# Optimization experiments

Hardware: AMD Instinct MI355X
Metric: run time of the kernel (lower is better)

The kernel has to match this reference:

```python
import jax, jax.numpy as jnp
import numpy as np

N_NODES = 100000
N_EDGES = 1000000
D = 128          # input_dim == hidden_dim (required: h = zeros_like(nh) accumulates src_nf)
OUT = 128
NUM_TYPES = 5


def setup_inputs() -> dict:
    key = jax.random.key(0)
    ks = jax.random.split(key, 7)
    nh = jax.random.normal(ks[0], (N_NODES, D), dtype=jnp.float32)
    edge_y = jax.random.randint(ks[1], (N_EDGES,), 0, NUM_TYPES, dtype=jnp.int64)
    edge_index = jax.random.randint(ks[2], (2, N_EDGES), 0, N_NODES, dtype=jnp.int64)
    # nn.Linear weights, scaled for numerical sanity
    W_nf = jax.random.normal(ks[3], (D, D), dtype=jnp.float32) * 0.08
    W_attn = jax.random.normal(ks[4], (1, 2 * D), dtype=jnp.float32) * 0.08
    W_out = jax.random.normal(ks[5], (OUT, 2 * D), dtype=jnp.float32) * 0.08
    b_out = jax.random.normal(ks[6], (OUT,), dtype=jnp.float32) * 0.01
    return {"nh": nh, "edge_y": edge_y, "edge_index": edge_index,
            "W_nf": W_nf, "W_attn": W_attn, "W_out": W_out, "b_out": b_out}


def reference(nh, edge_y, edge_index, W_nf, W_attn, W_out, b_out):
    n = nh.shape[0]
    src, dst = edge_index[0], edge_index[1]

    # nf_lin applied once per node, then gathered per edge (same math as
    # self.nf_lin(nh[src]) since Linear is per-row)
    nfl = nh @ W_nf.T                                  # [N, D]
    src_nf = nfl[src]                                  # [E, D]
    dst_nf = nfl[dst]                                  # [E, D]

    # attn(cat([src_nf, dst_nf])) == src_nf @ a_src + dst_nf @ a_dst
    a_src, a_dst = W_attn[0, :D], W_attn[0, D:]
    ef = src_nf @ a_src + dst_nf @ a_dst               # [E]
    ef = jnp.where(ef >= 0, ef, 0.2 * ef)              # LeakyReLU(0.2)

    # scatter_softmax per (edge_type, dst) group: the per-type loop with
    # scatter_softmax over dst is exactly a segment softmax over composite
    # segments seg = dst*5 + type; the summed per-type scatter_adds equal
    # one segment_sum over dst.
    seg = dst * NUM_TYPES + edge_y                     # [E]
    num_seg = n * NUM_TYPES
    m = jax.ops.segment_max(ef, seg, num_segments=num_seg)
    ex = jnp.exp(ef - m[seg])
    denom = jax.ops.segment_sum(ex, seg, num_segments=num_seg)
    alpha = ex / denom[seg]                            # [E]

    h = jax.ops.segment_sum(alpha[:, None] * src_nf, dst, num_segments=n)  # [N, D]

    nf = jnp.concatenate([nh, h], axis=-1) @ W_out.T + b_out
    return jax.nn.relu(nf)
```

## Files before the change

kernel.cpp:

```cpp
#include <hip/hip_runtime.h>

#define NTYPES 5
#define EPB 16384
#define BKSH 6
#define BKDST 64
#define CAP 2048

typedef _Float16 half8 __attribute__((ext_vector_type(8)));
typedef _Float16 half4v __attribute__((ext_vector_type(4)));
typedef float float4v __attribute__((ext_vector_type(4)));

__device__ __forceinline__ void stage_f32(
    _Float16* lds, const float* __restrict__ g, int rows, int stride4, int off4,
    int grow0, int nmax, int t)
{
  const float4* g4 = (const float4*)g;
  for (int i = t; i < rows * 32; i += 256) {
    int row = i >> 5, q = i & 31;
    float4 v = make_float4(0.f, 0.f, 0.f, 0.f);
    int gr = grow0 + row;
    if (gr < nmax) v = g4[(size_t)gr * stride4 + off4 + q];
    half4v hv = { (_Float16)v.x, (_Float16)v.y, (_Float16)v.z, (_Float16)v.w };
    int byte = row * 256 + ((q * 8) ^ ((row & 7) << 4));
    *(half4v*)((char*)lds + byte) = hv;
  }
}

__device__ __forceinline__ half8 frag_ld(const _Float16* lds, int row, int khw) {
  int byte = row * 256 + ((khw * 2) ^ ((row & 7) << 4));
  return *(const half8*)((const char*)lds + byte);
}

__device__ __forceinline__ half8 cvt8(float4 v0, float4 v1) {
  half8 a;
  a[0] = (_Float16)v0.x; a[1] = (_Float16)v0.y; a[2] = (_Float16)v0.z; a[3] = (_Float16)v0.w;
  a[4] = (_Float16)v1.x; a[5] = (_Float16)v1.y; a[6] = (_Float16)v1.z; a[7] = (_Float16)v1.w;
  return a;
}

__global__ __launch_bounds__(256) void k_gemm0(
    const float* __restrict__ nh, const float* __restrict__ Wnf,
    const float* __restrict__ Wattn,
    float* __restrict__ s_src, float* __restrict__ s_dst,
    _Float16* __restrict__ nfl, int n)
{
  __shared__ _Float16 wh[128 * 128];
  const int t = threadIdx.x, lane = t & 63, wv = t >> 6;
  const int r16 = lane & 15, g = lane >> 4;
  stage_f32(wh, Wnf, 128, 32, 0, 0, 1 << 30, t);
  float asrc[8], adst[8];
  #pragma unroll
  for (int nf = 0; nf < 8; ++nf) {
    asrc[nf] = Wattn[nf * 16 + r16];
    adst[nf] = Wattn[128 + nf * 16 + r16];
  }
  __syncthreads();
  const int nchunk = (n + 63) >> 6;
  for (int c = blockIdx.x; c < nchunk; c += gridDim.x) {
    const int base = c << 6;
    const int arow = base + wv * 16 + r16;
    const bool ok = arow < n;
    const float4* nh4 = (const float4*)(nh + (size_t)arow * 128);
    float4v acc[8];
    #pragma unroll
    for (int nf = 0; nf < 8; ++nf) acc[nf] = (float4v){0.f, 0.f, 0.f, 0.f};
    #pragma unroll
    for (int s = 0; s < 4; ++s) {
      float4 v0 = make_float4(0.f,0.f,0.f,0.f), v1 = v0;
      if (ok) { v0 = nh4[s * 8 + g * 2]; v1 = nh4[s * 8 + g * 2 + 1]; }
      half8 a = cvt8(v0, v1);
      #pragma unroll
      for (int nf = 0; nf < 8; ++nf)
        acc[nf] = __builtin_amdgcn_mfma_f32_16x16x32_f16(a, frag_ld(wh, nf * 16 + r16, s * 32 + g * 8), acc[nf], 0, 0, 0);
    }
    #pragma unroll
    for (int rr = 0; rr < 4; ++rr) {
      int node = base + wv * 16 + g * 4 + rr;
      if (node >= n) continue;
      size_t ro = (size_t)node * 128;
      #pragma unroll
      for (int nf = 0; nf < 8; ++nf) nfl[ro + nf * 16 + r16] = (_Float16)acc[nf][rr];
    }
    float ss[4] = {0.f, 0.f, 0.f, 0.f}, sd[4] = {0.f, 0.f, 0.f, 0.f};
    #pragma unroll
    for (int nf = 0; nf < 8; ++nf)
      #pragma unroll
      for (int rr = 0; rr < 4; ++rr) {
        ss[rr] = fmaf(acc[nf][rr], asrc[nf], ss[rr]);
        sd[rr] = fmaf(acc[nf][rr], adst[nf], sd[rr]);
      }
    #pragma unroll
    for (int m = 1; m <= 8; m <<= 1)
      #pragma unroll
      for (int rr = 0; rr < 4; ++rr) {
        ss[rr] += __shfl_xor(ss[rr], m);
        sd[rr] += __shfl_xor(sd[rr], m);
      }
    if (r16 == 0) {
      #pragma unroll
      for (int rr = 0; rr < 4; ++rr) {
        int node = base + wv * 16 + g * 4 + rr;
        if (node < n) { s_src[node] = ss[rr]; s_dst[node] = sd[rr]; }
      }
    }
  }
}

__global__ __launch_bounds__(256) void k_hist(
    const int* __restrict__ dsts, int* __restrict__ cnt, int e, int nbk, int nblk)
{
  __shared__ int hist[2048];
  const int t = threadIdx.x, b = blockIdx.x;
  for (int k = t; k < nbk; k += 256) hist[k] = 0;
  __syncthreads();
  const int i0 = b * EPB;
  const int iend = min(i0 + EPB, e);
  for (int i = i0 + t; i < iend; i += 256)
    atomicAdd(&hist[dsts[i] >> BKSH], 1);
  __syncthreads();
  for (int k = t; k < nbk; k += 256) cnt[k * nblk + b] = hist[k];
}

__global__ __launch_bounds__(256) void k_scan1(
    const int* __restrict__ deg, int* __restrict__ base, int* __restrict__ bsum, int n)
{
  __shared__ int ws[4];
  int t = threadIdx.x;
  int g0 = blockIdx.x * 1024 + t * 4;
  int4 v = make_int4(0, 0, 0, 0);
  if (g0 + 3 < n) v = *(const int4*)(deg + g0);
  else {
    if (g0     < n) v.x = deg[g0];
    if (g0 + 1 < n) v.y = deg[g0 + 1];
    if (g0 + 2 < n) v.z = deg[g0 + 2];
    if (g0 + 3 < n) v.w = deg[g0 + 3];
  }
  int s = v.x + v.y + v.z + v.w;
  int inc = s;
  #pragma unroll
  for (int d = 1; d < 64; d <<= 1) {
    int o = __shfl_up(inc, d);
    if ((t & 63) >= d) inc += o;
  }
  int wid = t >> 6;
  if ((t & 63) == 63) ws[wid] = inc;
  __syncthreads();
  int woff = 0;
  for (int w = 0; w < wid; ++w) woff += ws[w];
  int exc = woff + inc - s;
  if (g0 + 3 < n) {
    *(int4*)(base + g0) = make_int4(exc, exc + v.x, exc + v.x + v.y, exc + v.x + v.y + v.z);
  } else {
    if (g0     < n) base[g0]     = exc;
    if (g0 + 1 < n) base[g0 + 1] = exc + v.x;
    if (g0 + 2 < n) base[g0 + 2] = exc + v.x + v.y;
  }
  if (t == 255) bsum[blockIdx.x] = woff + inc;
}

__global__ __launch_bounds__(256) void k_scan2(
    const int* __restrict__ bsum, int* __restrict__ boff, int nb)
{
  __shared__ int ws[4];
  int t = threadIdx.x;
  int x = t < nb ? bsum[t] : 0;
  int inc = x;
  #pragma unroll
  for (int d = 1; d < 64; d <<= 1) {
    int o = __shfl_up(inc, d);
    if ((t & 63) >= d) inc += o;
  }
  int wid = t >> 6;
  if ((t & 63) == 63) ws[wid] = inc;
  __syncthreads();
  int woff = 0;
  for (int w = 0; w < wid; ++w) woff += ws[w];
  if (t < nb) boff[t] = woff + inc - x;
}

__global__ __launch_bounds__(256) void k_scan3(
    int* __restrict__ base, const int* __restrict__ boff, int n)
{
  int i = blockIdx.x * 256 + threadIdx.x;
  if (i < n) base[i] += boff[i >> 10];
}

__global__ __launch_bounds__(256) void k_scatter2(
    const int* __restrict__ ei, const int* __restrict__ ey,
    const int* __restrict__ cnt_s, unsigned* __restrict__ rec,
    int e, int nbk, int nblk)
{
  __shared__ int cur[2048];
  const int t = threadIdx.x, b = blockIdx.x;
  for (int k = t; k < nbk; k += 256) cur[k] = cnt_s[k * nblk + b];
  __syncthreads();
  const int i0 = b * EPB;
  const int iend = min(i0 + EPB, e);
  for (int i = i0 + t; i < iend; i += 256) {
    int s = ei[i], d = ei[e + i], ty = ey[i];
    int pos = atomicAdd(&cur[d >> BKSH], 1);
    rec[pos] = (unsigned)s | ((unsigned)ty << 17) | ((unsigned)(d & (BKDST - 1)) << 20);
  }
}

__global__ __launch_bounds__(256) void k_agg2(
    const unsigned* __restrict__ rec, const int* __restrict__ cnt_s,
    const float* __restrict__ s_src, const float* __restrict__ s_dst,
    const _Float16* __restrict__ nfl, _Float16* __restrict__ h,
    int n, int e, int nbk, int nblk)
{
  __shared__ unsigned ord[CAP];
  __shared__ float efl[CAP];
  __shared__ int dcnt[BKDST];
  __shared__ int dbase[BKDST + 1];
  __shared__ float sdl[BKDST];
  const int t = threadIdx.x;
  const int k = blockIdx.x;
  const int d0 = k << BKSH;
  const int ndst = min(BKDST, n - d0);
  const int bs = cnt_s[k * nblk];
  const int be = (k + 1 < nbk) ? cnt_s[(k + 1) * nblk] : e;
  const int cnt = be - bs;
  if (t < BKDST) {
    dcnt[t] = 0;
    if (t < ndst) sdl[t] = s_dst[d0 + t];
  }
  __syncthreads();
  const int g = t >> 4, l = t & 15;

  if (cnt <= CAP) {
    for (int i = t; i < cnt; i += 256)
      atomicAdd(&dcnt[(rec[bs + i] >> 20) & (BKDST - 1)], 1);
    __syncthreads();
    if (t < BKDST) {
      int v = dcnt[t];
      int inc = v;
      #pragma unroll
      for (int dd = 1; dd < 64; dd <<= 1) {
        int o = __shfl_up(inc, dd);
        if (t >= dd) inc += o;
      }
      dbase[t] = inc - v;
      dcnt[t]  = inc - v;
      if (t == BKDST - 1) dbase[BKDST] = inc;
    }
    __syncthreads();
    for (int i = t; i < cnt; i += 256) {
      unsigned p = rec[bs + i];
      int pos = atomicAdd(&dcnt[(p >> 20) & (BKDST - 1)], 1);
      ord[pos] = p;
    }
    __syncthreads();
    for (int i = t; i < cnt; i += 256) {
      unsigned p = ord[i];
      float ef = s_src[p & 0x1FFFF] + sdl[(p >> 20) & (BKDST - 1)];
      efl[i] = ef >= 0.f ? ef : 0.2f * ef;
    }
    __syncthreads();
    for (int di = g; di < ndst; di += 16) {
      int s0 = dbase[di], deg = dbase[di + 1] - s0;
      float acc[8] = {0.f, 0.f, 0.f, 0.f, 0.f, 0.f, 0.f, 0.f};
      if (deg > 0) {
        float mx[NTYPES];
        #pragma unroll
        for (int tt = 0; tt < NTYPES; ++tt) mx[tt] = -1e30f;
        for (int j0 = 0; j0 < deg; j0 += 16) {
          int jj = j0 + l;
          bool ok = jj < deg;
          float ef = ok ? efl[s0 + jj] : -1e30f;
          int ty = ok ? (int)((ord[s0 + jj] >> 17) & 7) : 7;
          #pragma unroll
          for (int tt = 0; tt < NTYPES; ++tt) {
            float v = (ty == tt) ? ef : -1e30f;
            v = fmaxf(v, __shfl_xor(v, 1)); v = fmaxf(v, __shfl_xor(v, 2));
            v = fmaxf(v, __shfl_xor(v, 4)); v = fmaxf(v, __shfl_xor(v, 8));
            mx[tt] = fmaxf(mx[tt], v);
          }
        }
        float sm[NTYPES];
        #pragma unroll
        for (int tt = 0; tt < NTYPES; ++tt) sm[tt] = 0.f;
        for (int j0 = 0; j0 < deg; j0 += 16) {
          int jj = j0 + l;
          bool ok = jj < deg;
          int ty = ok ? (int)((ord[s0 + jj] >> 17) & 7) : 7;
          float ex = ok ? __expf(efl[s0 + jj] - mx[ty]) : 0.f;
          if (ok) efl[s0 + jj] = ex;
          #pragma unroll
          for (int tt = 0; tt < NTYPES; ++tt) {
            float v = (ty == tt) ? ex : 0.f;
            v += __shfl_xor(v, 1); v += __shfl_xor(v, 2);
            v += __shfl_xor(v, 4); v += __shfl_xor(v, 8);
            sm[tt] += v;
          }
        }
        float rsm[NTYPES];
        #pragma unroll
        for (int tt = 0; tt < NTYPES; ++tt) rsm[tt] = sm[tt] > 0.f ? 1.f / sm[tt] : 0.f;
        int j = 0;
        for (; j + 2 <= deg; j += 2) {
          unsigned p0 = ord[s0 + j], p1 = ord[s0 + j + 1];
          float a0 = efl[s0 + j] * rsm[(p0 >> 17) & 7];
          float a1 = efl[s0 + j + 1] * rsm[(p1 >> 17) & 7];
          half8 x0 = *(const half8*)(nfl + (size_t)(p0 & 0x1FFFF) * 128 + l * 8);
          half8 x1 = *(const half8*)(nfl + (size_t)(p1 & 0x1FFFF) * 128 + l * 8);
          #pragma unroll
          for (int kk = 0; kk < 8; ++kk) acc[kk] = fmaf(a0, (float)x0[kk], acc[kk]);
          #pragma unroll
          for (int kk = 0; kk < 8; ++kk) acc[kk] = fmaf(a1, (float)x1[kk], acc[kk]);
        }
        if (j < deg) {
          unsigned p0 = ord[s0 + j];
          float a0 = efl[s0 + j] * rsm[(p0 >> 17) & 7];
          half8 x0 = *(const half8*)(nfl + (size_t)(p0 & 0x1FFFF) * 128 + l * 8);
          #pragma unroll
          for (int kk = 0; kk < 8; ++kk) acc[kk] = fmaf(a0, (float)x0[kk], acc[kk]);
        }
      }
      half8 hv;
      #pragma unroll
      for (int kk = 0; kk < 8; ++kk) hv[kk] = (_Float16)acc[kk];
      *(half8*)(h + (size_t)(d0 + di) * 128 + l * 8) = hv;
    }
  } else {
    const int gb = (t & 63) & 48;
    for (int di = g; di < ndst; di += 16) {
      float mx[NTYPES], sm[NTYPES];
      #pragma unroll
      for (int tt = 0; tt < NTYPES; ++tt) { mx[tt] = -1e30f; sm[tt] = 0.f; }
      for (int j0 = 0; j0 < cnt; j0 += 16) {
        int jj = j0 + l;
        unsigned p = (jj < cnt) ? rec[bs + jj] : 0xFFFFFFFFu;
        bool mine = (p != 0xFFFFFFFFu) && (int)((p >> 20) & (BKDST - 1)) == di;
        float ef = -1e30f; int ty = 7;
        if (mine) {
          ef = s_src[p & 0x1FFFF] + sdl[di];
          ef = ef >= 0.f ? ef : 0.2f * ef;
          ty = (p >> 17) & 7;
        }
        #pragma unroll
        for (int tt = 0; tt < NTYPES; ++tt) {
          float v = (mine && ty == tt) ? ef : -1e30f;
          v = fmaxf(v, __shfl_xor(v, 1)); v = fmaxf(v, __shfl_xor(v, 2));
          v = fmaxf(v, __shfl_xor(v, 4)); v = fmaxf(v, __shfl_xor(v, 8));
          mx[tt] = fmaxf(mx[tt], v);
        }
      }
      for (int j0 = 0; j0 < cnt; j0 += 16) {
        int jj = j0 + l;
        unsigned p = (jj < cnt) ? rec[bs + jj] : 0xFFFFFFFFu;
        bool mine = (p != 0xFFFFFFFFu) && (int)((p >> 20) & (BKDST - 1)) == di;
        float ex = 0.f; int ty = 7;
        if (mine) {
          float ef = s_src[p & 0x1FFFF] + sdl[di];
          ef = ef >= 0.f ? ef : 0.2f * ef;
          ty = (p >> 17) & 7;
          ex = __expf(ef - mx[ty]);
        }
        #pragma unroll
        for (int tt = 0; tt < NTYPES; ++tt) {
          float v = (ty == tt) ? ex : 0.f;
          v += __shfl_xor(v, 1); v += __shfl_xor(v, 2);
          v += __shfl_xor(v, 4); v += __shfl_xor(v, 8);
          sm[tt] += v;
        }
      }
      float rsm[NTYPES];
      #pragma unroll
      for (int tt = 0; tt < NTYPES; ++tt) rsm[tt] = sm[tt] > 0.f ? 1.f / sm[tt] : 0.f;
      float acc[8] = {0.f, 0.f, 0.f, 0.f, 0.f, 0.f, 0.f, 0.f};
      for (int j0 = 0; j0 < cnt; j0 += 16) {
        int jj = j0 + l;
        unsigned p = (jj < cnt) ? rec[bs + jj] : 0xFFFFFFFFu;
        bool mine = (p != 0xFFFFFFFFu) && (int)((p >> 20) & (BKDST - 1)) == di;
        float al = 0.f;
        if (mine) {
          float ef = s_src[p & 0x1FFFF] + sdl[di];
          ef = ef >= 0.f ? ef : 0.2f * ef;
          int ty = (p >> 17) & 7;
          al = __expf(ef - mx[ty]) * rsm[ty];
        }
        unsigned pv = mine ? p : 0xFFFFFFFFu;
        for (int jj2 = 0; jj2 < 16; ++jj2) {
          unsigned pp = __shfl(pv, gb + jj2);
          float aa = __shfl(al, gb + jj2);
          if (pp != 0xFFFFFFFFu) {
            half8 x = *(const half8*)(nfl + (size_t)(pp & 0x1FFFF) * 128 + l * 8);
            #pragma unroll
            for (int kk = 0; kk < 8; ++kk) acc[kk] = fmaf(aa, (float)x[kk], acc[kk]);
          }
        }
      }
      half8 hv;
      #pragma unroll
      for (int kk = 0; kk < 8; ++kk) hv[kk] = (_Float16)acc[kk];
      *(half8*)(h + (size_t)(d0 + di) * 128 + l * 8) = hv;
    }
  }
}

__global__ __launch_bounds__(256) void k_gemmO(
    const float* __restrict__ nh, const _Float16* __restrict__ hbuf,
    const float* __restrict__ Wout, const float* __restrict__ bias,
    float* __restrict__ out, int n)
{
  __shared__ _Float16 w1[64 * 128], w2[64 * 128];
  const int t = threadIdx.x, lane = t & 63, wv = t >> 6;
  const int r16 = lane & 15, g = lane >> 4;
  const int jhalf = blockIdx.x & 1;
  stage_f32(w1, Wout, 64, 64, 0,  jhalf * 64, 1 << 30, t);
  stage_f32(w2, Wout, 64, 64, 32, jhalf * 64, 1 << 30, t);
  float bv[4];
  #pragma unroll
  for (int nf = 0; nf < 4; ++nf) bv[nf] = bias[jhalf * 64 + nf * 16 + r16];
  __syncthreads();
  const int nchunk = (n + 63) >> 6;
  for (int c = blockIdx.x >> 1; c < nchunk; c += gridDim.x >> 1) {
    const int base = c << 6;
    const int arow = base + wv * 16 + r16;
    const bool ok = arow < n;
    const float4* nh4 = (const float4*)(nh + (size_t)arow * 128);
    const _Float16* hb = hbuf + (size_t)arow * 128;
    float4v acc[4];
    #pragma unroll
    for (int nf = 0; nf < 4; ++nf) acc[nf] = (float4v){0.f, 0.f, 0.f, 0.f};
    #pragma unroll
    for (int s = 0; s < 4; ++s) {
      float4 v0 = make_float4(0.f,0.f,0.f,0.f), v1 = v0;
      half8 a2 = {};
      if (ok) {
        v0 = nh4[s * 8 + g * 2];
        v1 = nh4[s * 8 + g * 2 + 1];
        a2 = *(const half8*)(hb + s * 32 + g * 8);
      }
      half8 a1 = cvt8(v0, v1);
      #pragma unroll
      for (int nf = 0; nf < 4; ++nf) {
        acc[nf] = __builtin_amdgcn_mfma_f32_16x16x32_f16(a1, frag_ld(w1, nf * 16 + r16, s * 32 + g * 8), acc[nf], 0, 0, 0);
        acc[nf] = __builtin_amdgcn_mfma_f32_16x16x32_f16(a2, frag_ld(w2, nf * 16 + r16, s * 32 + g * 8), acc[nf], 0, 0, 0);
      }
    }
    #pragma unroll
    for (int rr = 0; rr < 4; ++rr) {
      int node = base + wv * 16 + g * 4 + rr;
      if (node >= n) continue;
      #pragma unroll
      for (int nf = 0; nf < 4; ++nf)
        out[(size_t)node * 128 + jhalf * 64 + nf * 16 + r16] = fmaxf(acc[nf][rr] + bv[nf], 0.f);
    }
  }
}

extern "C" void kernel_launch(void* const* d_in, const int* in_sizes, int n_in,
                              void* d_out, int out_size, void* d_ws, size_t ws_size,
                              hipStream_t stream) {
  const float* nh     = (const float*)d_in[0];
  const int*   edge_y = (const int*)d_in[1];
  const int*   ei     = (const int*)d_in[2];
  const float* W_nf   = (const float*)d_in[3];
  const float* W_attn = (const float*)d_in[4];
  const float* W_out  = (const float*)d_in[5];
  const float* b_out  = (const float*)d_in[6];
  float* out = (float*)d_out;
  const int n = in_sizes[0] / 128;
  const int e = in_sizes[1];
  const int nbk  = (n + BKDST - 1) >> BKSH;
  const int nblk = (e + EPB - 1) / EPB;
  const int ncnt = nbk * nblk;
  const int nb2  = (ncnt + 1023) / 1024;

  _Float16* nfl_h = (_Float16*)d_ws;
  _Float16* h_h   = nfl_h + (size_t)n * 128;
  float* s_src = (float*)(h_h + (size_t)n * 128);
  float* s_dst = s_src + n;
  int*   cnt   = (int*)(s_dst + n);
  int*   bsum  = cnt + ncnt;
  int*   boff  = bsum + 256;
  unsigned* rec = (unsigned*)(boff + 256);

  k_gemm0<<<1280, 256, 0, stream>>>(nh, W_nf, W_attn, s_src, s_dst, nfl_h, n);
  k_hist<<<nblk, 256, 0, stream>>>(ei + e, cnt, e, nbk, nblk);
  k_scan1<<<nb2, 256, 0, stream>>>(cnt, cnt, bsum, ncnt);
  k_scan2<<<1, 256, 0, stream>>>(bsum, boff, nb2);
  k_scan3<<<(ncnt + 255) / 256, 256, 0, stream>>>(cnt, boff, ncnt);
  k_scatter2<<<nblk, 256, 0, stream>>>(ei, edge_y, cnt, rec, e, nbk, nblk);
  k_agg2<<<nbk, 256, 0, stream>>>(rec, cnt, s_src, s_dst, nfl_h, h_h, n, e, nbk, nblk);
  k_gemmO<<<2560, 256, 0, stream>>>(nh, h_h, W_out, b_out, out, n);
}
```

Measured before the change: 181.0 us.

## Fuse output GEMM into gemm0 and aggregation, dropping k_gemmO and h buffer

The nh half of the output projection (nh @ W_out[:, :128]^T + bias) is now computed inside k_gemm0 alongside nfl and stored as a half-precision t1 buffer. The h @ W_out[:, 128:]^T half is computed in k_agg2 directly from an LDS tile of the aggregated h rows, then added to t1 with a ReLU and written to out. k_gemm0 also prefetches the next chunk's nh rows into registers and runs on fewer blocks. This removes the separate output GEMM kernel and the global h write and read-back, at the cost of a t1 round trip in fp16 (extra rounding), more LDS per block, and W_out being reloaded from global by every aggregation block.

```diff
diff --git a/kernel.cpp b/kernel.cpp
--- a/kernel.cpp
+++ b/kernel.cpp
@@ -38,40 +38,69 @@
   return a;
 }
 
+struct A8 { float4 v[8]; };
+__device__ __forceinline__ A8 loadA8(const float* __restrict__ nh, int arow, int n, int g) {
+  A8 r;
+  const float4* p = (const float4*)(nh + (size_t)arow * 128);
+  bool ok = arow < n;
+  float4 z = make_float4(0.f, 0.f, 0.f, 0.f);
+  #pragma unroll
+  for (int s = 0; s < 4; ++s) {
+    r.v[2 * s]     = ok ? p[s * 8 + g * 2]     : z;
+    r.v[2 * s + 1] = ok ? p[s * 8 + g * 2 + 1] : z;
+  }
+  return r;
+}
+
 __global__ __launch_bounds__(256) void k_gemm0(
     const float* __restrict__ nh, const float* __restrict__ Wnf,
-    const float* __restrict__ Wattn,
+    const float* __restrict__ Wout, const float* __restrict__ Wattn,
+    const float* __restrict__ bias,
     float* __restrict__ s_src, float* __restrict__ s_dst,
-    _Float16* __restrict__ nfl, int n)
+    _Float16* __restrict__ nfl, _Float16* __restrict__ t1, int n)
 {
   __shared__ _Float16 wh[128 * 128];
+  __shared__ _Float16 wo[128 * 128];
   const int t = threadIdx.x, lane = t & 63, wv = t >> 6;
   const int r16 = lane & 15, g = lane >> 4;
   stage_f32(wh, Wnf, 128, 32, 0, 0, 1 << 30, t);
-  float asrc[8], adst[8];
+  stage_f32(wo, Wout, 128, 64, 0, 0, 1 << 30, t);
+  float asrc[8], adst[8], bv[8];
   #pragma unroll
   for (int nf = 0; nf < 8; ++nf) {
     asrc[nf] = Wattn[nf * 16 + r16];
     adst[nf] = Wattn[128 + nf * 16 + r16];
+    bv[nf]   = bias[nf * 16 + r16];
   }
   __syncthreads();
   const int nchunk = (n + 63) >> 6;
-  for (int c = blockIdx.x; c < nchunk; c += gridDim.x) {
+  const int gstride = gridDim.x;
+  int c = blockIdx.x;
+  A8 cur;
+  if (c < nchunk) cur = loadA8(nh, (c << 6) + wv * 16 + r16, n, g);
+  for (; c < nchunk; c += gstride) {
     const int base = c << 6;
-    const int arow = base + wv * 16 + r16;
-    const bool ok = arow < n;
-    const float4* nh4 = (const float4*)(nh + (size_t)arow * 128);
-    float4v acc[8];
-    #pragma unroll
-    for (int nf = 0; nf < 8; ++nf) acc[nf] = (float4v){0.f, 0.f, 0.f, 0.f};
+    int cn = c + gstride;
+    A8 nxt;
+    #pragma unroll
+    for (int q = 0; q < 8; ++q) nxt.v[q] = make_float4(0.f, 0.f, 0.f, 0.f);
+    if (cn < nchunk) nxt = loadA8(nh, (cn << 6) + wv * 16 + r16, n, g);
+
+    float4v accN[8], accT[8];
+    #pragma unroll
+    for (int nf = 0; nf < 8; ++nf) {
+      accN[nf] = (float4v){0.f, 0.f, 0.f, 0.f};
+      accT[nf] = (float4v){0.f, 0.f, 0.f, 0.f};
+    }
     #pragma unroll
     for (int s = 0; s < 4; ++s) {
-      float4 v0 = make_float4(0.f,0.f,0.f,0.f), v1 = v0;
-      if (ok) { v0 = nh4[s * 8 + g * 2]; v1 = nh4[s * 8 + g * 2 + 1]; }
-      half8 a = cvt8(v0, v1);
+      half8 a = cvt8(cur.v[2 * s], cur.v[2 * s + 1]);
       #pragma unroll
       for (int nf = 0; nf < 8; ++nf)
-        acc[nf] = __builtin_amdgcn_mfma_f32_16x16x32_f16(a, frag_ld(wh, nf * 16 + r16, s * 32 + g * 8), acc[nf], 0, 0, 0);
+        accN[nf] = __builtin_amdgcn_mfma_f32_16x16x32_f16(a, frag_ld(wh, nf * 16 + r16, s * 32 + g * 8), accN[nf], 0, 0, 0);
+      #pragma unroll
+      for (int nf = 0; nf < 8; ++nf)
+        accT[nf] = __builtin_amdgcn_mfma_f32_16x16x32_f16(a, frag_ld(wo, nf * 16 + r16, s * 32 + g * 8), accT[nf], 0, 0, 0);
     }
     #pragma unroll
     for (int rr = 0; rr < 4; ++rr) {
@@ -79,15 +108,18 @@
       if (node >= n) continue;
       size_t ro = (size_t)node * 128;
       #pragma unroll
-      for (int nf = 0; nf < 8; ++nf) nfl[ro + nf * 16 + r16] = (_Float16)acc[nf][rr];
+      for (int nf = 0; nf < 8; ++nf) {
+        nfl[ro + nf * 16 + r16] = (_Float16)accN[nf][rr];
+        t1[ro + nf * 16 + r16]  = (_Float16)(accT[nf][rr] + bv[nf]);
+      }
     }
     float ss[4] = {0.f, 0.f, 0.f, 0.f}, sd[4] = {0.f, 0.f, 0.f, 0.f};
     #pragma unroll
     for (int nf = 0; nf < 8; ++nf)
       #pragma unroll
       for (int rr = 0; rr < 4; ++rr) {
-        ss[rr] = fmaf(acc[nf][rr], asrc[nf], ss[rr]);
-        sd[rr] = fmaf(acc[nf][rr], adst[nf], sd[rr]);
+        ss[rr] = fmaf(accN[nf][rr], asrc[nf], ss[rr]);
+        sd[rr] = fmaf(accN[nf][rr], adst[nf], sd[rr]);
       }
     #pragma unroll
     for (int m = 1; m <= 8; m <<= 1)
@@ -103,6 +135,7 @@
         if (node < n) { s_src[node] = ss[rr]; s_dst[node] = sd[rr]; }
       }
     }
+    cur = nxt;
   }
 }
 
@@ -206,11 +239,13 @@
 __global__ __launch_bounds__(256) void k_agg2(
     const unsigned* __restrict__ rec, const int* __restrict__ cnt_s,
     const float* __restrict__ s_src, const float* __restrict__ s_dst,
-    const _Float16* __restrict__ nfl, _Float16* __restrict__ h,
+    const _Float16* __restrict__ nfl, const _Float16* __restrict__ t1,
+    const float* __restrict__ Wout, float* __restrict__ out,
     int n, int e, int nbk, int nblk)
 {
   __shared__ unsigned ord[CAP];
   __shared__ float efl[CAP];
+  __shared__ _Float16 htile[BKDST * 128];
   __shared__ int dcnt[BKDST];
   __shared__ int dbase[BKDST + 1];
   __shared__ float sdl[BKDST];
@@ -224,6 +259,15 @@
   if (t < BKDST) {
     dcnt[t] = 0;
     if (t < ndst) sdl[t] = s_dst[d0 + t];
+  }
+  if (ndst < BKDST) {
+    for (int i = t; i < BKDST * 16; i += 256) {
+      int row = i >> 4;
+      if (row >= ndst) {
+        half8 z = {};
+        *(half8*)((char*)htile + row * 256 + (((i & 15) * 16) ^ ((row & 7) << 4))) = z;
+      }
+    }
   }
   __syncthreads();
   const int g = t >> 4, l = t & 15;
@@ -320,7 +364,7 @@
       half8 hv;
       #pragma unroll
       for (int kk = 0; kk < 8; ++kk) hv[kk] = (_Float16)acc[kk];
-      *(half8*)(h + (size_t)(d0 + di) * 128 + l * 8) = hv;
+      *(half8*)((char*)htile + di * 256 + ((l * 16) ^ ((di & 7) << 4))) = hv;
     }
   } else {
     const int gb = (t & 63) & 48;
@@ -394,61 +438,50 @@
       half8 hv;
       #pragma unroll
       for (int kk = 0; kk < 8; ++kk) hv[kk] = (_Float16)acc[kk];
-      *(half8*)(h + (size_t)(d0 + di) * 128 + l * 8) = hv;
-    }
-  }
-}
-
-__global__ __launch_bounds__(256) void k_gemmO(
-    const float* __restrict__ nh, const _Float16* __restrict__ hbuf,
-    const float* __restrict__ Wout, const float* __restrict__ bias,
-    float* __restrict__ out, int n)
-{
-  __shared__ _Float16 w1[64 * 128], w2[64 * 128];
-  const int t = threadIdx.x, lane = t & 63, wv = t >> 6;
-  const int r16 = lane & 15, g = lane >> 4;
-  const int jhalf = blockIdx.x & 1;
-  stage_f32(w1, Wout, 64, 64, 0,  jhalf * 64, 1 << 30, t);
-  stage_f32(w2, Wout, 64, 64, 32, jhalf * 64, 1 << 30, t);
-  float bv[4];
-  #pragma unroll
-  for (int nf = 0; nf < 4; ++nf) bv[nf] = bias[jhalf * 64 + nf * 16 + r16];
-  __syncthreads();
-  const int nchunk = (n + 63) >> 6;
-  for (int c = blockIdx.x >> 1; c < nchunk; c += gridDim.x >> 1) {
-    const int base = c << 6;
-    const int arow = base + wv * 16 + r16;
-    const bool ok = arow < n;
-    const float4* nh4 = (const float4*)(nh + (size_t)arow * 128);
-    const _Float16* hb = hbuf + (size_t)arow * 128;
-    float4v acc[4];
-    #pragma unroll
-    for (int nf = 0; nf < 4; ++nf) acc[nf] = (float4v){0.f, 0.f, 0.f, 0.f};
-    #pragma unroll
-    for (int s = 0; s < 4; ++s) {
-      float4 v0 = make_float4(0.f,0.f,0.f,0.f), v1 = v0;
-      half8 a2 = {};
-      if (ok) {
-        v0 = nh4[s * 8 + g * 2];
-        v1 = nh4[s * 8 + g * 2 + 1];
-        a2 = *(const half8*)(hb + s * 32 + g * 8);
-      }
-      half8 a1 = cvt8(v0, v1);
-      #pragma unroll
-      for (int nf = 0; nf < 4; ++nf) {
-        acc[nf] = __builtin_amdgcn_mfma_f32_16x16x32_f16(a1, frag_ld(w1, nf * 16 + r16, s * 32 + g * 8), acc[nf], 0, 0, 0);
-        acc[nf] = __builtin_amdgcn_mfma_f32_16x16x32_f16(a2, frag_ld(w2, nf * 16 + r16, s * 32 + g * 8), acc[nf], 0, 0, 0);
-      }
-    }
-    #pragma unroll
-    for (int rr = 0; rr < 4; ++rr) {
-      int node = base + wv * 16 + g * 4 + rr;
-      if (node >= n) continue;
-      #pragma unroll
-      for (int nf = 0; nf < 4; ++nf)
-        out[(size_t)node * 128 + jhalf * 64 + nf * 16 + r16] = fmaxf(acc[nf][rr] + bv[nf], 0.f);
-    }
-  }
+      *(half8*)((char*)htile + di * 256 + ((l * 16) ^ ((di & 7) << 4))) = hv;
+    }
+  }
+  __syncthreads();
+
+  const int wv = t >> 6, lane = t & 63;
+  const int r16 = lane & 15, gq = lane >> 4;
+  float4v accB[4][2];
+  #pragma unroll
+  for (int m = 0; m < 4; ++m) {
+    accB[m][0] = (float4v){0.f, 0.f, 0.f, 0.f};
+    accB[m][1] = (float4v){0.f, 0.f, 0.f, 0.f};
+  }
+  #pragma unroll
+  for (int s = 0; s < 4; ++s) {
+    half8 bf0, bf1;
+    {
+      int col0 = wv * 32 + r16;
+      const float4* wr0 = (const float4*)(Wout + (size_t)col0 * 256 + 128);
+      bf0 = cvt8(wr0[s * 8 + gq * 2], wr0[s * 8 + gq * 2 + 1]);
+      const float4* wr1 = (const float4*)(Wout + (size_t)(col0 + 16) * 256 + 128);
+      bf1 = cvt8(wr1[s * 8 + gq * 2], wr1[s * 8 + gq * 2 + 1]);
+    }
+    #pragma unroll
+    for (int m = 0; m < 4; ++m) {
+      half8 a = frag_ld(htile, m * 16 + r16, s * 32 + gq * 8);
+      accB[m][0] = __builtin_amdgcn_mfma_f32_16x16x32_f16(a, bf0, accB[m][0], 0, 0, 0);
+      accB[m][1] = __builtin_amdgcn_mfma_f32_16x16x32_f16(a, bf1, accB[m][1], 0, 0, 0);
+    }
+  }
+  #pragma unroll
+  for (int m = 0; m < 4; ++m)
+    #pragma unroll
+    for (int nf = 0; nf < 2; ++nf) {
+      int col = wv * 32 + nf * 16 + r16;
+      #pragma unroll
+      for (int rr = 0; rr < 4; ++rr) {
+        int row = m * 16 + gq * 4 + rr;
+        if (row < ndst) {
+          size_t o = (size_t)(d0 + row) * 128 + col;
+          out[o] = fmaxf(accB[m][nf][rr] + (float)t1[o], 0.f);
+        }
+      }
+    }
 }
 
 extern "C" void kernel_launch(void* const* d_in, const int* in_sizes, int n_in,
@@ -470,20 +503,21 @@
   const int nb2  = (ncnt + 1023) / 1024;
 
   _Float16* nfl_h = (_Float16*)d_ws;
-  _Float16* h_h   = nfl_h + (size_t)n * 128;
-  float* s_src = (float*)(h_h + (size_t)n * 128);
+  _Float16* t1_h  = nfl_h + (size_t)n * 128;
+  float* s_src = (float*)(t1_h + (size_t)n * 128);
   float* s_dst = s_src + n;
   int*   cnt   = (int*)(s_dst + n);
   int*   bsum  = cnt + ncnt;
   int*   boff  = bsum + 256;
   unsigned* rec = (unsigned*)(boff + 256);
 
-  k_gemm0<<<1280, 256, 0, stream>>>(nh, W_nf, W_attn, s_src, s_dst, nfl_h, n);
+  k_gemm0<<<512, 256, 0, stream>>>(nh, W_nf, W_out, W_attn, b_out,
+                                   s_src, s_dst, nfl_h, t1_h, n);
   k_hist<<<nblk, 256, 0, stream>>>(ei + e, cnt, e, nbk, nblk);
   k_scan1<<<nb2, 256, 0, stream>>>(cnt, cnt, bsum, ncnt);
   k_scan2<<<1, 256, 0, stream>>>(bsum, boff, nb2);
   k_scan3<<<(ncnt + 255) / 256, 256, 0, stream>>>(cnt, boff, ncnt);
   k_scatter2<<<nblk, 256, 0, stream>>>(ei, edge_y, cnt, rec, e, nbk, nblk);
-  k_agg2<<<nbk, 256, 0, stream>>>(rec, cnt, s_src, s_dst, nfl_h, h_h, n, e, nbk, nblk);
-  k_gemmO<<<2560, 256, 0, stream>>>(nh, h_h, W_out, b_out, out, n);
-}
+  k_agg2<<<nbk, 256, 0, stream>>>(rec, cnt, s_src, s_dst, nfl_h, t1_h,
+                                  W_out, out, n, e, nbk, nblk);
+}
```

New measurement: 192.7 us. 6.5% more time.

## Cache fp16 copy of nh, prefetch GEMM rows, unroll aggregation by four

Applied to the files above, without the earlier changes.

k_gemm0 now writes an fp16 copy of nh to the workspace, and k_gemmO reads that copy instead of the fp32 input, halving its nh read traffic. Both GEMM kernels software-prefetch the next chunk's A rows into registers while computing the current chunk. k_agg2's gather loop is unrolled from two to four edges to keep more loads in flight, and k_gemmO's grid is halved. The cost is an extra 25MB fp16 write in gemm0 and higher register pressure from the prefetch buffers.

```diff
diff --git a/kernel.cpp b/kernel.cpp
--- a/kernel.cpp
+++ b/kernel.cpp
@@ -38,11 +38,25 @@
   return a;
 }
 
+struct A8 { float4 v[8]; };
+__device__ __forceinline__ A8 loadA8(const float* __restrict__ nh, int arow, int n, int g) {
+  A8 r;
+  const float4* p = (const float4*)(nh + (size_t)arow * 128);
+  bool ok = arow < n;
+  float4 z = make_float4(0.f, 0.f, 0.f, 0.f);
+  #pragma unroll
+  for (int s = 0; s < 4; ++s) {
+    r.v[2 * s]     = ok ? p[s * 8 + g * 2]     : z;
+    r.v[2 * s + 1] = ok ? p[s * 8 + g * 2 + 1] : z;
+  }
+  return r;
+}
+
 __global__ __launch_bounds__(256) void k_gemm0(
     const float* __restrict__ nh, const float* __restrict__ Wnf,
     const float* __restrict__ Wattn,
     float* __restrict__ s_src, float* __restrict__ s_dst,
-    _Float16* __restrict__ nfl, int n)
+    _Float16* __restrict__ nfl, _Float16* __restrict__ nh16, int n)
 {
   __shared__ _Float16 wh[128 * 128];
   const int t = threadIdx.x, lane = t & 63, wv = t >> 6;
@@ -56,19 +70,26 @@
   }
   __syncthreads();
   const int nchunk = (n + 63) >> 6;
-  for (int c = blockIdx.x; c < nchunk; c += gridDim.x) {
+  const int gstride = gridDim.x;
+  int c = blockIdx.x;
+  A8 cur;
+  if (c < nchunk) cur = loadA8(nh, (c << 6) + wv * 16 + r16, n, g);
+  for (; c < nchunk; c += gstride) {
     const int base = c << 6;
+    int cn = c + gstride;
+    A8 nxt;
+    #pragma unroll
+    for (int q = 0; q < 8; ++q) nxt.v[q] = make_float4(0.f, 0.f, 0.f, 0.f);
+    if (cn < nchunk) nxt = loadA8(nh, (cn << 6) + wv * 16 + r16, n, g);
+
     const int arow = base + wv * 16 + r16;
-    const bool ok = arow < n;
-    const float4* nh4 = (const float4*)(nh + (size_t)arow * 128);
     float4v acc[8];
     #pragma unroll
     for (int nf = 0; nf < 8; ++nf) acc[nf] = (float4v){0.f, 0.f, 0.f, 0.f};
     #pragma unroll
     for (int s = 0; s < 4; ++s) {
-      float4 v0 = make_float4(0.f,0.f,0.f,0.f), v1 = v0;
-      if (ok) { v0 = nh4[s * 8 + g * 2]; v1 = nh4[s * 8 + g * 2 + 1]; }
-      half8 a = cvt8(v0, v1);
+      half8 a = cvt8(cur.v[2 * s], cur.v[2 * s + 1]);
+      if (arow < n) *(half8*)(nh16 + (size_t)arow * 128 + s * 32 + g * 8) = a;
       #pragma unroll
       for (int nf = 0; nf < 8; ++nf)
         acc[nf] = __builtin_amdgcn_mfma_f32_16x16x32_f16(a, frag_ld(wh, nf * 16 + r16, s * 32 + g * 8), acc[nf], 0, 0, 0);
@@ -103,6 +124,7 @@
         if (node < n) { s_src[node] = ss[rr]; s_dst[node] = sd[rr]; }
       }
     }
+    cur = nxt;
   }
 }
 
@@ -298,18 +320,27 @@
         #pragma unroll
         for (int tt = 0; tt < NTYPES; ++tt) rsm[tt] = sm[tt] > 0.f ? 1.f / sm[tt] : 0.f;
         int j = 0;
-        for (; j + 2 <= deg; j += 2) {
-          unsigned p0 = ord[s0 + j], p1 = ord[s0 + j + 1];
-          float a0 = efl[s0 + j] * rsm[(p0 >> 17) & 7];
+        for (; j + 4 <= deg; j += 4) {
+          unsigned p0 = ord[s0 + j],     p1 = ord[s0 + j + 1];
+          unsigned p2 = ord[s0 + j + 2], p3 = ord[s0 + j + 3];
+          float a0 = efl[s0 + j]     * rsm[(p0 >> 17) & 7];
           float a1 = efl[s0 + j + 1] * rsm[(p1 >> 17) & 7];
+          float a2 = efl[s0 + j + 2] * rsm[(p2 >> 17) & 7];
+          float a3 = efl[s0 + j + 3] * rsm[(p3 >> 17) & 7];
           half8 x0 = *(const half8*)(nfl + (size_t)(p0 & 0x1FFFF) * 128 + l * 8);
           half8 x1 = *(const half8*)(nfl + (size_t)(p1 & 0x1FFFF) * 128 + l * 8);
+          half8 x2 = *(const half8*)(nfl + (size_t)(p2 & 0x1FFFF) * 128 + l * 8);
+          half8 x3 = *(const half8*)(nfl + (size_t)(p3 & 0x1FFFF) * 128 + l * 8);
           #pragma unroll
           for (int kk = 0; kk < 8; ++kk) acc[kk] = fmaf(a0, (float)x0[kk], acc[kk]);
           #pragma unroll
           for (int kk = 0; kk < 8; ++kk) acc[kk] = fmaf(a1, (float)x1[kk], acc[kk]);
-        }
-        if (j < deg) {
+          #pragma unroll
+          for (int kk = 0; kk < 8; ++kk) acc[kk] = fmaf(a2, (float)x2[kk], acc[kk]);
+          #pragma unroll
+          for (int kk = 0; kk < 8; ++kk) acc[kk] = fmaf(a3, (float)x3[kk], acc[kk]);
+        }
+        for (; j < deg; ++j) {
           unsigned p0 = ord[s0 + j];
           float a0 = efl[s0 + j] * rsm[(p0 >> 17) & 7];
           half8 x0 = *(const half8*)(nfl + (size_t)(p0 & 0x1FFFF) * 128 + l * 8);
@@ -400,7 +431,7 @@
 }
 
 __global__ __launch_bounds__(256) void k_gemmO(
-    const float* __restrict__ nh, const _Float16* __restrict__ hbuf,
+    const _Float16* __restrict__ nh16, const _Float16* __restrict__ hbuf,
     const float* __restrict__ Wout, const float* __restrict__ bias,
     float* __restrict__ out, int n)
 {
@@ -415,29 +446,40 @@
   for (int nf = 0; nf < 4; ++nf) bv[nf] = bias[jhalf * 64 + nf * 16 + r16];
   __syncthreads();
   const int nchunk = (n + 63) >> 6;
-  for (int c = blockIdx.x >> 1; c < nchunk; c += gridDim.x >> 1) {
+  const int gstride = gridDim.x >> 1;
+  int c = blockIdx.x >> 1;
+  half8 c1[4], c2[4];
+  if (c < nchunk) {
+    int arow = (c << 6) + wv * 16 + r16;
+    bool ok = arow < n;
+    #pragma unroll
+    for (int s = 0; s < 4; ++s) {
+      c1[s] = ok ? *(const half8*)(nh16 + (size_t)arow * 128 + s * 32 + g * 8) : (half8){};
+      c2[s] = ok ? *(const half8*)(hbuf + (size_t)arow * 128 + s * 32 + g * 8) : (half8){};
+    }
+  }
+  for (; c < nchunk; c += gstride) {
     const int base = c << 6;
-    const int arow = base + wv * 16 + r16;
-    const bool ok = arow < n;
-    const float4* nh4 = (const float4*)(nh + (size_t)arow * 128);
-    const _Float16* hb = hbuf + (size_t)arow * 128;
+    int cn = c + gstride;
+    half8 n1[4] = {}, n2[4] = {};
+    if (cn < nchunk) {
+      int arow = (cn << 6) + wv * 16 + r16;
+      bool ok = arow < n;
+      #pragma unroll
+      for (int s = 0; s < 4; ++s) {
+        n1[s] = ok ? *(const half8*)(nh16 + (size_t)arow * 128 + s * 32 + g * 8) : (half8){};
+        n2[s] = ok ? *(const half8*)(hbuf + (size_t)arow * 128 + s * 32 + g * 8) : (half8){};
+      }
+    }
     float4v acc[4];
     #pragma unroll
     for (int nf = 0; nf < 4; ++nf) acc[nf] = (float4v){0.f, 0.f, 0.f, 0.f};
     #pragma unroll
     for (int s = 0; s < 4; ++s) {
-      float4 v0 = make_float4(0.f,0.f,0.f,0.f), v1 = v0;
-      half8 a2 = {};
-      if (ok) {
-        v0 = nh4[s * 8 + g * 2];
-        v1 = nh4[s * 8 + g * 2 + 1];
-        a2 = *(const half8*)(hb + s * 32 + g * 8);
-      }
-      half8 a1 = cvt8(v0, v1);
       #pragma unroll
       for (int nf = 0; nf < 4; ++nf) {
-        acc[nf] = __builtin_amdgcn_mfma_f32_16x16x32_f16(a1, frag_ld(w1, nf * 16 + r16, s * 32 + g * 8), acc[nf], 0, 0, 0);
-        acc[nf] = __builtin_amdgcn_mfma_f32_16x16x32_f16(a2, frag_ld(w2, nf * 16 + r16, s * 32 + g * 8), acc[nf], 0, 0, 0);
+        acc[nf] = __builtin_amdgcn_mfma_f32_16x16x32_f16(c1[s], frag_ld(w1, nf * 16 + r16, s * 32 + g * 8), acc[nf], 0, 0, 0);
+        acc[nf] = __builtin_amdgcn_mfma_f32_16x16x32_f16(c2[s], frag_ld(w2, nf * 16 + r16, s * 32 + g * 8), acc[nf], 0, 0, 0);
       }
     }
     #pragma unroll
@@ -448,6 +490,8 @@
       for (int nf = 0; nf < 4; ++nf)
         out[(size_t)node * 128 + jhalf * 64 + nf * 16 + r16] = fmaxf(acc[nf][rr] + bv[nf], 0.f);
     }
+    #pragma unroll
+    for (int s = 0; s < 4; ++s) { c1[s] = n1[s]; c2[s] = n2[s]; }
   }
 }
 
@@ -470,7 +514,8 @@
   const int nb2  = (ncnt + 1023) / 1024;
 
   _Float16* nfl_h = (_Float16*)d_ws;
-  _Float16* h_h   = nfl_h + (size_t)n * 128;
+  _Float16* nh16  = nfl_h + (size_t)n * 128;
+  _Float16* h_h   = nh16 + (size_t)n * 128;
   float* s_src = (float*)(h_h + (size_t)n * 128);
   float* s_dst = s_src + n;
   int*   cnt   = (int*)(s_dst + n);
@@ -478,12 +523,12 @@
   int*   boff  = bsum + 256;
   unsigned* rec = (unsigned*)(boff + 256);
 
-  k_gemm0<<<1280, 256, 0, stream>>>(nh, W_nf, W_attn, s_src, s_dst, nfl_h, n);
+  k_gemm0<<<1280, 256, 0, stream>>>(nh, W_nf, W_attn, s_src, s_dst, nfl_h, nh16, n);
   k_hist<<<nblk, 256, 0, stream>>>(ei + e, cnt, e, nbk, nblk);
   k_scan1<<<nb2, 256, 0, stream>>>(cnt, cnt, bsum, ncnt);
   k_scan2<<<1, 256, 0, stream>>>(bsum, boff, nb2);
   k_scan3<<<(ncnt + 255) / 256, 256, 0, stream>>>(cnt, boff, ncnt);
   k_scatter2<<<nblk, 256, 0, stream>>>(ei, edge_y, cnt, rec, e, nbk, nblk);
   k_agg2<<<nbk, 256, 0, stream>>>(rec, cnt, s_src, s_dst, nfl_h, h_h, n, e, nbk, nblk);
-  k_gemmO<<<2560, 256, 0, stream>>>(nh, h_h, W_out, b_out, out, n);
-}
+  k_gemmO<<<1280, 256, 0, stream>>>(nh16, h_h, W_out, b_out, out, n);
+}
```

Measured after the change: 192.9 us. 6.6% more time.
